# Performance work log

Measured on AMD Instinct MI355X. Metric: run time of the kernel, lower is better.

Reference implementation:

```python
import jax, jax.numpy as jnp
import numpy as np

# Synaptic (snntorch) constants: alpha = exp(-dt/tau_s), beta = exp(-dt/tau_m)
DT, TAU_S, TAU_M = 1.0, 5.0, 10.0
ALPHA = float(np.exp(-DT / TAU_S))
BETA = float(np.exp(-DT / TAU_M))
THRESH = 1.0


def heaviside(u):
    return (u > 0).astype(u.dtype)


def setup_inputs() -> dict:
    key = jax.random.key(0)
    k1, k2 = jax.random.split(key)
    T, B, D1, D2 = 128, 256, 1024, 512
    inp = jax.random.uniform(k1, (T, B, D1), dtype=jnp.float32)
    # kaiming_normal_ on [d2, d1] (fan_in = d1), then * mu (=1.0)
    w = jax.random.normal(k2, (D2, D1), dtype=jnp.float32) * np.float32(np.sqrt(2.0 / D1))
    return {"input": inp, "weight": w}


def reference(input, weight):
    T, B = input.shape[0], input.shape[1]
    D2 = weight.shape[0]
    # step i (i=1..T-1) consumes F.linear(input[i-1], W); batch all GEMMs at once
    cur = jnp.einsum('tbi,oi->tbo', input[:-1], weight)  # [T-1, B, D2]

    def step(carry, c):
        syn, mem = carry
        reset = heaviside(mem - THRESH)          # spike from previous membrane
        syn = ALPHA * syn + c                    # synaptic current decay + drive
        mem = (BETA * mem + syn) * (1.0 - reset)  # zero-reset membrane update
        spk = heaviside(mem - THRESH)
        return (syn, mem), (spk, mem, syn)

    zeros = jnp.zeros((B, D2), input.dtype)
    _, (spk, V, I) = jax.lax.scan(step, (zeros, zeros), cur)

    z0 = jnp.zeros((1, B, D2), input.dtype)  # outputs at t=0 stay zero
    output = jnp.concatenate([z0, spk], axis=0)
    V = jnp.concatenate([z0, V], axis=0)
    I = jnp.concatenate([z0, I], axis=0)
    return output, V, I
```

## Files before the change

kernel.cpp:

```cpp
#include <hip/hip_runtime.h>
#include <cstddef>

#define TT 128
#define BB 256
#define D1 1024
#define D2 512
#define SS (BB * D2)
#define MM (127 * BB)

#define ALPHA 0.8187307530779818f
#define BETA  0.9048374180359595f

typedef _Float16 half8 __attribute__((ext_vector_type(8)));
typedef _Float16 half4v __attribute__((ext_vector_type(4)));
typedef float floatx16 __attribute__((ext_vector_type(16)));

__global__ __launch_bounds__(256) void convert_w(const float* __restrict__ W,
                                                 _Float16* __restrict__ Whi,
                                                 _Float16* __restrict__ Wlo) {
    const int i = (blockIdx.x * 256 + threadIdx.x) * 4;
    float4 w = *(const float4*)(W + i);
    half4v hi, lo;
    hi.x = (_Float16)w.x; lo.x = (_Float16)((w.x - (float)hi.x) * 2048.0f);
    hi.y = (_Float16)w.y; lo.y = (_Float16)((w.y - (float)hi.y) * 2048.0f);
    hi.z = (_Float16)w.z; lo.z = (_Float16)((w.z - (float)hi.z) * 2048.0f);
    hi.w = (_Float16)w.w; lo.w = (_Float16)((w.w - (float)hi.w) * 2048.0f);
    *(half4v*)(Whi + i) = hi;
    *(half4v*)(Wlo + i) = lo;
}

#define BM 64
#define BN 256
#define BK 32
#define LDH 48

__global__ __launch_bounds__(256, 2) void gemm_mfma(const float* __restrict__ A,
                                                    const _Float16* __restrict__ Whi,
                                                    const _Float16* __restrict__ Wlo,
                                                    float* __restrict__ C) {
    __shared__ _Float16 Ah[BM * LDH];
    __shared__ _Float16 Al[BM * LDH];
    __shared__ _Float16 Wh[BN * LDH];
    __shared__ _Float16 Wl[BN * LDH];

    const int tid = threadIdx.x;
    const int lane = tid & 63;
    const int wv = tid >> 6;
    const int bm = blockIdx.x * BM;
    const int bn = blockIdx.y * BN;

    const int arow = tid >> 2;
    const int kch = (tid & 3) * 8;

    const int m_ = lane & 31;
    const int q = lane >> 5;

    floatx16 accm[2][2], accl[2][2];
#pragma unroll
    for (int i = 0; i < 2; ++i)
#pragma unroll
        for (int j = 0; j < 2; ++j) {
            accm[i][j] = (floatx16)0.0f;
            accl[i][j] = (floatx16)0.0f;
        }

    const float* Abase = A + (size_t)(bm + arow) * D1 + kch;

    for (int k0 = 0; k0 < D1; k0 += BK) {
        float4 a0 = *(const float4*)(Abase + k0);
        float4 a1 = *(const float4*)(Abase + k0 + 4);
        half8 wh[4], wl[4];
#pragma unroll
        for (int p = 0; p < 4; ++p) {
            const int wr = bn + p * 64 + arow;
            wh[p] = *(const half8*)(Whi + wr * D1 + k0 + kch);
            wl[p] = *(const half8*)(Wlo + wr * D1 + k0 + kch);
        }

        __syncthreads();

        float av[8] = {a0.x, a0.y, a0.z, a0.w, a1.x, a1.y, a1.z, a1.w};
        half8 ah, al;
#pragma unroll
        for (int j = 0; j < 8; ++j) {
            _Float16 h = (_Float16)av[j];
            ah[j] = h;
            al[j] = (_Float16)((av[j] - (float)h) * 2048.0f);
        }
        *(half8*)&Ah[arow * LDH + kch] = ah;
        *(half8*)&Al[arow * LDH + kch] = al;
#pragma unroll
        for (int p = 0; p < 4; ++p) {
            *(half8*)&Wh[(p * 64 + arow) * LDH + kch] = wh[p];
            *(half8*)&Wl[(p * 64 + arow) * LDH + kch] = wl[p];
        }
        __syncthreads();

#pragma unroll
        for (int kk = 0; kk < BK; kk += 16) {
            const int ko = kk + q * 8;
            half8 a_hi[2], a_lo[2], b_hi[2], b_lo[2];
#pragma unroll
            for (int mb = 0; mb < 2; ++mb) {
                a_hi[mb] = *(const half8*)&Ah[(mb * 32 + m_) * LDH + ko];
                a_lo[mb] = *(const half8*)&Al[(mb * 32 + m_) * LDH + ko];
            }
#pragma unroll
            for (int nb = 0; nb < 2; ++nb) {
                b_hi[nb] = *(const half8*)&Wh[(wv * 64 + nb * 32 + m_) * LDH + ko];
                b_lo[nb] = *(const half8*)&Wl[(wv * 64 + nb * 32 + m_) * LDH + ko];
            }
#pragma unroll
            for (int mb = 0; mb < 2; ++mb)
#pragma unroll
                for (int nb = 0; nb < 2; ++nb) {
                    accm[mb][nb] = __builtin_amdgcn_mfma_f32_32x32x16_f16(
                        a_hi[mb], b_hi[nb], accm[mb][nb], 0, 0, 0);
                    accl[mb][nb] = __builtin_amdgcn_mfma_f32_32x32x16_f16(
                        a_hi[mb], b_lo[nb], accl[mb][nb], 0, 0, 0);
                    accl[mb][nb] = __builtin_amdgcn_mfma_f32_32x32x16_f16(
                        a_lo[mb], b_hi[nb], accl[mb][nb], 0, 0, 0);
                }
        }
    }

#pragma unroll
    for (int mb = 0; mb < 2; ++mb)
#pragma unroll
        for (int nb = 0; nb < 2; ++nb) {
            const int n = bn + wv * 64 + nb * 32 + m_;
#pragma unroll
            for (int reg = 0; reg < 16; ++reg) {
                const int row = (reg & 3) + 8 * (reg >> 2) + 4 * q;
                const int m = bm + mb * 32 + row;
                C[m * D2 + n] = accm[mb][nb][reg] + accl[mb][nb][reg] * (1.0f / 2048.0f);
            }
        }
}

__global__ __launch_bounds__(256) void scan_kernel(float* __restrict__ out) {
    const int j = blockIdx.x * 256 + threadIdx.x;
    float* spk = out;
    float* V = out + TT * SS;
    float* I = out + 2 * TT * SS;

    spk[j] = 0.0f;
    V[j] = 0.0f;
    I[j] = 0.0f;

    float syn = 0.0f, mem = 0.0f;

#define STEP(tt, cc)                                     \
    {                                                    \
        const float reset = (mem > 1.0f) ? 1.0f : 0.0f;  \
        syn = ALPHA * syn + (cc);                        \
        mem = (BETA * mem + syn) * (1.0f - reset);       \
        const int idx = (tt) * SS + j;                   \
        spk[idx] = (mem > 1.0f) ? 1.0f : 0.0f;           \
        V[idx] = mem;                                    \
        I[idx] = syn;                                    \
    }

    float c0 = I[1 * SS + j];
    float c1 = I[2 * SS + j];
    float c2 = I[3 * SS + j];
    float c3 = I[4 * SS + j];

    int t = 1;
    for (; t <= 117; t += 4) {
        const float n0 = I[(t + 4) * SS + j];
        const float n1 = I[(t + 5) * SS + j];
        const float n2 = I[(t + 6) * SS + j];
        const float n3 = I[(t + 7) * SS + j];
        STEP(t + 0, c0);
        STEP(t + 1, c1);
        STEP(t + 2, c2);
        STEP(t + 3, c3);
        c0 = n0; c1 = n1; c2 = n2; c3 = n3;
    }
    {
        const float n0 = I[125 * SS + j];
        const float n1 = I[126 * SS + j];
        const float n2 = I[127 * SS + j];
        STEP(121, c0);
        STEP(122, c1);
        STEP(123, c2);
        STEP(124, c3);
        STEP(125, n0);
        STEP(126, n1);
        STEP(127, n2);
    }
#undef STEP
}

extern "C" void kernel_launch(void* const* d_in, const int* in_sizes, int n_in,
                              void* d_out, int out_size, void* d_ws, size_t ws_size,
                              hipStream_t stream) {
    const float* input = (const float*)d_in[0];
    const float* weight = (const float*)d_in[1];
    float* out = (float*)d_out;

    _Float16* Whi = (_Float16*)(out + SS);
    _Float16* Wlo = Whi + (size_t)D2 * D1;

    float* Cdst = out + (size_t)2 * TT * SS + SS;

    convert_w<<<dim3((D2 * D1 / 4) / 256), dim3(256), 0, stream>>>(weight, Whi, Wlo);
    gemm_mfma<<<dim3(MM / BM, D2 / BN), dim3(256), 0, stream>>>(input, Whi, Wlo, Cdst);
    scan_kernel<<<dim3(SS / 256), dim3(256), 0, stream>>>(out);
}
```

Before: 406.5 us.

## Load weight fragments directly into registers, drop W LDS staging, deepen scan prefetch

The GEMM no longer stages the hi/lo fp16 weight tiles through shared memory. Each wave loads its B fragments straight from global memory into registers, software-pipelined one half-tile ahead, which removes LDS writes, reads and footprint and raises possible occupancy. The A-tile LDS row stride is reduced from 48 to 40. The scan kernel prefetches 8 timesteps instead of 4 to hide more load latency. In exchange, B loads are now strided 16-byte global reads per lane that rely on L2/cache reuse across blocks, and the scan uses more registers.

```diff
diff --git a/kernel.cpp b/kernel.cpp
--- a/kernel.cpp
+++ b/kernel.cpp
@@ -32,7 +32,7 @@
 #define BM 64
 #define BN 256
 #define BK 32
-#define LDH 48
+#define LDH 40
 
 __global__ __launch_bounds__(256, 2) void gemm_mfma(const float* __restrict__ A,
                                                     const _Float16* __restrict__ Whi,
@@ -40,8 +40,6 @@
                                                     float* __restrict__ C) {
     __shared__ _Float16 Ah[BM * LDH];
     __shared__ _Float16 Al[BM * LDH];
-    __shared__ _Float16 Wh[BN * LDH];
-    __shared__ _Float16 Wl[BN * LDH];
 
     const int tid = threadIdx.x;
     const int lane = tid & 63;
@@ -55,6 +53,15 @@
     const int m_ = lane & 31;
     const int q = lane >> 5;
 
+    const _Float16* WhiB[2];
+    const _Float16* WloB[2];
+#pragma unroll
+    for (int nb = 0; nb < 2; ++nb) {
+        const size_t off = (size_t)(bn + wv * 64 + nb * 32 + m_) * D1 + q * 8;
+        WhiB[nb] = Whi + off;
+        WloB[nb] = Wlo + off;
+    }
+
     floatx16 accm[2][2], accl[2][2];
 #pragma unroll
     for (int i = 0; i < 2; ++i)
@@ -66,15 +73,22 @@
 
     const float* Abase = A + (size_t)(bm + arow) * D1 + kch;
 
+    half8 bh0[2], bl0[2];
+#pragma unroll
+    for (int nb = 0; nb < 2; ++nb) {
+        bh0[nb] = *(const half8*)(WhiB[nb]);
+        bl0[nb] = *(const half8*)(WloB[nb]);
+    }
+
     for (int k0 = 0; k0 < D1; k0 += BK) {
         float4 a0 = *(const float4*)(Abase + k0);
         float4 a1 = *(const float4*)(Abase + k0 + 4);
-        half8 wh[4], wl[4];
-#pragma unroll
-        for (int p = 0; p < 4; ++p) {
-            const int wr = bn + p * 64 + arow;
-            wh[p] = *(const half8*)(Whi + wr * D1 + k0 + kch);
-            wl[p] = *(const half8*)(Wlo + wr * D1 + k0 + kch);
+
+        half8 bh1[2], bl1[2];
+#pragma unroll
+        for (int nb = 0; nb < 2; ++nb) {
+            bh1[nb] = *(const half8*)(WhiB[nb] + k0 + 16);
+            bl1[nb] = *(const half8*)(WloB[nb] + k0 + 16);
         }
 
         __syncthreads();
@@ -89,37 +103,54 @@
         }
         *(half8*)&Ah[arow * LDH + kch] = ah;
         *(half8*)&Al[arow * LDH + kch] = al;
-#pragma unroll
-        for (int p = 0; p < 4; ++p) {
-            *(half8*)&Wh[(p * 64 + arow) * LDH + kch] = wh[p];
-            *(half8*)&Wl[(p * 64 + arow) * LDH + kch] = wl[p];
-        }
         __syncthreads();
 
-#pragma unroll
-        for (int kk = 0; kk < BK; kk += 16) {
-            const int ko = kk + q * 8;
-            half8 a_hi[2], a_lo[2], b_hi[2], b_lo[2];
+        {
+            const int ko = q * 8;
+            half8 a_hi[2], a_lo[2];
 #pragma unroll
             for (int mb = 0; mb < 2; ++mb) {
                 a_hi[mb] = *(const half8*)&Ah[(mb * 32 + m_) * LDH + ko];
                 a_lo[mb] = *(const half8*)&Al[(mb * 32 + m_) * LDH + ko];
             }
 #pragma unroll
-            for (int nb = 0; nb < 2; ++nb) {
-                b_hi[nb] = *(const half8*)&Wh[(wv * 64 + nb * 32 + m_) * LDH + ko];
-                b_lo[nb] = *(const half8*)&Wl[(wv * 64 + nb * 32 + m_) * LDH + ko];
-            }
-#pragma unroll
             for (int mb = 0; mb < 2; ++mb)
 #pragma unroll
                 for (int nb = 0; nb < 2; ++nb) {
                     accm[mb][nb] = __builtin_amdgcn_mfma_f32_32x32x16_f16(
-                        a_hi[mb], b_hi[nb], accm[mb][nb], 0, 0, 0);
-                    accl[mb][nb] = __builtin_amdgcn_mfma_f32_32x32x16_f16(
-                        a_hi[mb], b_lo[nb], accl[mb][nb], 0, 0, 0);
-                    accl[mb][nb] = __builtin_amdgcn_mfma_f32_32x32x16_f16(
-                        a_lo[mb], b_hi[nb], accl[mb][nb], 0, 0, 0);
+                        a_hi[mb], bh0[nb], accm[mb][nb], 0, 0, 0);
+                    accl[mb][nb] = __builtin_amdgcn_mfma_f32_32x32x16_f16(
+                        a_hi[mb], bl0[nb], accl[mb][nb], 0, 0, 0);
+                    accl[mb][nb] = __builtin_amdgcn_mfma_f32_32x32x16_f16(
+                        a_lo[mb], bh0[nb], accl[mb][nb], 0, 0, 0);
+                }
+        }
+
+        const int kn = (k0 + BK < D1) ? (k0 + BK) : 0;
+#pragma unroll
+        for (int nb = 0; nb < 2; ++nb) {
+            bh0[nb] = *(const half8*)(WhiB[nb] + kn);
+            bl0[nb] = *(const half8*)(WloB[nb] + kn);
+        }
+
+        {
+            const int ko = 16 + q * 8;
+            half8 a_hi[2], a_lo[2];
+#pragma unroll
+            for (int mb = 0; mb < 2; ++mb) {
+                a_hi[mb] = *(const half8*)&Ah[(mb * 32 + m_) * LDH + ko];
+                a_lo[mb] = *(const half8*)&Al[(mb * 32 + m_) * LDH + ko];
+            }
+#pragma unroll
+            for (int mb = 0; mb < 2; ++mb)
+#pragma unroll
+                for (int nb = 0; nb < 2; ++nb) {
+                    accm[mb][nb] = __builtin_amdgcn_mfma_f32_32x32x16_f16(
+                        a_hi[mb], bh1[nb], accm[mb][nb], 0, 0, 0);
+                    accl[mb][nb] = __builtin_amdgcn_mfma_f32_32x32x16_f16(
+                        a_hi[mb], bl1[nb], accl[mb][nb], 0, 0, 0);
+                    accl[mb][nb] = __builtin_amdgcn_mfma_f32_32x32x16_f16(
+                        a_lo[mb], bh1[nb], accl[mb][nb], 0, 0, 0);
                 }
         }
     }
@@ -133,7 +164,7 @@
             for (int reg = 0; reg < 16; ++reg) {
                 const int row = (reg & 3) + 8 * (reg >> 2) + 4 * q;
                 const int m = bm + mb * 32 + row;
-                C[m * D2 + n] = accm[mb][nb][reg] + accl[mb][nb][reg] * (1.0f / 2048.0f);
+                C[(size_t)m * D2 + n] = accm[mb][nb][reg] + accl[mb][nb][reg] * (1.0f / 2048.0f);
             }
         }
 }
@@ -161,34 +192,28 @@
         I[idx] = syn;                                    \
     }
 
-    float c0 = I[1 * SS + j];
-    float c1 = I[2 * SS + j];
-    float c2 = I[3 * SS + j];
-    float c3 = I[4 * SS + j];
+    float c[8];
+#pragma unroll
+    for (int i = 0; i < 8; ++i) c[i] = I[(1 + i) * SS + j];
 
     int t = 1;
-    for (; t <= 117; t += 4) {
-        const float n0 = I[(t + 4) * SS + j];
-        const float n1 = I[(t + 5) * SS + j];
-        const float n2 = I[(t + 6) * SS + j];
-        const float n3 = I[(t + 7) * SS + j];
-        STEP(t + 0, c0);
-        STEP(t + 1, c1);
-        STEP(t + 2, c2);
-        STEP(t + 3, c3);
-        c0 = n0; c1 = n1; c2 = n2; c3 = n3;
+    for (; t <= 105; t += 8) {
+        float nx[8];
+#pragma unroll
+        for (int i = 0; i < 8; ++i) nx[i] = I[(t + 8 + i) * SS + j];
+#pragma unroll
+        for (int i = 0; i < 8; ++i) STEP(t + i, c[i]);
+#pragma unroll
+        for (int i = 0; i < 8; ++i) c[i] = nx[i];
     }
     {
-        const float n0 = I[125 * SS + j];
-        const float n1 = I[126 * SS + j];
-        const float n2 = I[127 * SS + j];
-        STEP(121, c0);
-        STEP(122, c1);
-        STEP(123, c2);
-        STEP(124, c3);
-        STEP(125, n0);
-        STEP(126, n1);
-        STEP(127, n2);
+        float nx[7];
+#pragma unroll
+        for (int i = 0; i < 7; ++i) nx[i] = I[(121 + i) * SS + j];
+#pragma unroll
+        for (int i = 0; i < 8; ++i) STEP(113 + i, c[i]);
+#pragma unroll
+        for (int i = 0; i < 7; ++i) STEP(121 + i, nx[i]);
     }
 #undef STEP
 }
```

After: 483.9 us. 19.0% more time.
